# Kernel tuning notes

Measured on AMD Instinct MI355X. Metric: run time of the kernel, lower is better.

Reference implementation:

```python
import jax, jax.numpy as jnp
import numpy as np

B, S, H = 32, 1, 1024            # decode: one query token per sequence
NH, HD = 16, 64                  # num_heads, head_dim
BS = 16                          # cache block size
MAX_KV = 2048                    # max sequence length in cache
BLOCKS_PER_SEQ = MAX_KV // BS    # 128
NUM_BLOCKS = B * BLOCKS_PER_SEQ  # 4096 physical blocks
SCALE = HD ** -0.5


def setup_inputs() -> dict:
    key = jax.random.key(0)
    ks = jax.random.split(key, 8)
    hidden_states = jax.random.normal(ks[0], (B, S, H), jnp.float32) * 0.02
    # kv_cache[0] = key cache, kv_cache[1] = value cache; paged layout
    kv_cache = jax.random.normal(ks[1], (2, NUM_BLOCKS, BS, NH, HD), jnp.float32) * 0.02
    # each sequence owns a contiguous run of physical blocks (valid block table)
    block_tables = jnp.arange(NUM_BLOCKS, dtype=jnp.int32).reshape(B, BLOCKS_PER_SEQ)
    seq_lens = jax.random.randint(ks[2], (B,), 1, MAX_KV + 1, dtype=jnp.int32)
    w_attn = jax.random.normal(ks[3], (H, 3 * H), jnp.float32) * 0.02
    b_attn = jax.random.normal(ks[4], (3 * H,), jnp.float32) * 0.02
    w_proj = jax.random.normal(ks[5], (H, H), jnp.float32) * 0.02
    b_proj = jax.random.normal(ks[6], (H,), jnp.float32) * 0.02
    return {"hidden_states": hidden_states, "kv_cache": kv_cache,
            "block_tables": block_tables, "seq_lens": seq_lens,
            "w_attn": w_attn, "b_attn": b_attn,
            "w_proj": w_proj, "b_proj": b_proj}


def reference(hidden_states, kv_cache, block_tables, seq_lens,
              w_attn, b_attn, w_proj, b_proj):
    # qkv projection (c_attn); only q is consumed by the paged-attention decode
    qkv = hidden_states @ w_attn + b_attn                      # [B, S, 3H]
    q = qkv[..., :H].reshape(B, S, NH, HD)                     # [B, 1, NH, HD]

    # block-table gather of paged KV cache
    # kv_cache[0][block_tables]: [B, BLOCKS_PER_SEQ, BS, NH, HD]
    keys = kv_cache[0][block_tables].reshape(B, MAX_KV, NH, HD)
    vals = kv_cache[1][block_tables].reshape(B, MAX_KV, NH, HD)

    scores = jnp.einsum('bsnd,bknd->bnsk', q, keys) * SCALE    # [B, NH, S, MAX_KV]
    valid = jnp.arange(MAX_KV)[None, :] < seq_lens[:, None]    # [B, MAX_KV]
    scores = jnp.where(valid[:, None, None, :], scores, -jnp.inf)
    probs = jax.nn.softmax(scores, axis=-1)

    attn = jnp.einsum('bnsk,bknd->bsnd', probs, vals).reshape(B, S, H)
    return attn @ w_proj + b_proj                              # [B, S, H]
```

## Files before the change

kernel.cpp:

```cpp
#include <hip/hip_runtime.h>
#include <hip/hip_bf16.h>

#define BATCH 32
#define HID 1024
#define NH 16
#define HD 64
#define BS 16
#define MAX_KV 2048
#define BPS 128
#define NUM_BLOCKS 4096
#define SCALE 0.125f

#define SPLITS 16
#define CHUNK 128
#define KSPLIT 16
#define KCHUNK (HID / KSPLIT)

__global__ __launch_bounds__(256) void init_kernel(
    const float* __restrict__ b_attn, const float* __restrict__ b_proj,
    float* __restrict__ q, float* __restrict__ out)
{
    const int i = blockIdx.x * 256 + threadIdx.x;
    const int col = i & (HID - 1);
    q[i]   = b_attn[col];
    out[i] = b_proj[col];
}

__global__ __launch_bounds__(256) void gemv_kernel(
    const float* __restrict__ x,
    const float* __restrict__ w,
    float* __restrict__ y,
    int wstride)
{
    const int colg = blockIdx.x;
    const int kz = blockIdx.y;
    const int tid = threadIdx.x, wave = tid >> 6, lane = tid & 63;
    const int col = colg * 64 + lane;

    __shared__ __align__(16) float s_x[BATCH * KCHUNK];
    for (int i = tid; i < BATCH * KCHUNK; i += 256) {
        const int bb = i >> 6, kk = i & (KCHUNK - 1);
        s_x[i] = x[bb * HID + kz * KCHUNK + kk];
    }
    __syncthreads();

    const int b0 = wave * 8;
    float acc[8];
    #pragma unroll
    for (int b = 0; b < 8; ++b) acc[b] = 0.f;

    const float4* s_x4 = reinterpret_cast<const float4*>(s_x);
    const float* wp = w + (size_t)(kz * KCHUNK) * wstride + col;
    #pragma unroll
    for (int jb = 0; jb < KCHUNK / 4; ++jb) {
        const float wv0 = wp[(size_t)(jb * 4 + 0) * wstride];
        const float wv1 = wp[(size_t)(jb * 4 + 1) * wstride];
        const float wv2 = wp[(size_t)(jb * 4 + 2) * wstride];
        const float wv3 = wp[(size_t)(jb * 4 + 3) * wstride];
        #pragma unroll
        for (int b = 0; b < 8; ++b) {
            const float4 xv = s_x4[(b0 + b) * (KCHUNK / 4) + jb];
            acc[b] += xv.x * wv0 + xv.y * wv1 + xv.z * wv2 + xv.w * wv3;
        }
    }
    #pragma unroll
    for (int b = 0; b < 8; ++b)
        atomicAdd(&y[(size_t)(b0 + b) * HID + col], acc[b]);
}

__global__ __launch_bounds__(256) void attn_split_kernel(
    const float* __restrict__ q,
    const float* __restrict__ kv,
    const int* __restrict__ block_tables,
    const int* __restrict__ seq_lens,
    float* __restrict__ part)
{
    const int h = blockIdx.x, b = blockIdx.y, s = blockIdx.z;
    const int n = seq_lens[b];
    const int p0 = s * CHUNK;
    if (p0 >= n) return;
    const int cnt = min(n - p0, CHUNK);

    const int tid = threadIdx.x, wave = tid >> 6, lane = tid & 63;
    const int pos_sub = lane >> 4;
    const int d4 = lane & 15;

    float* my_part = part + ((size_t)(b * NH + h) * SPLITS + s) * (HD + 2);

    __shared__ float s_sc[CHUNK];
    __shared__ int   s_bt[CHUNK / BS];
    __shared__ float s_redm[4], s_redl[4];
    __shared__ float s_part[4 * HD];

    if (tid < CHUNK / BS) s_bt[tid] = block_tables[b * BPS + s * (CHUNK / BS) + tid];
    float4 qv = *reinterpret_cast<const float4*>(
        q + (size_t)(b * NH + h) * HD + d4 * 4);
    qv.x *= SCALE; qv.y *= SCALE; qv.z *= SCALE; qv.w *= SCALE;
    __syncthreads();

    const size_t v_off = (size_t)NUM_BLOCKS * BS * NH * HD;

    for (int base = wave * 16; base < cnt; base += 64) {
        float sc[4];
        #pragma unroll
        for (int u = 0; u < 4; ++u) {
            const int p = base + 4 * pos_sub + u;
            sc[u] = 0.f;
            if (p < cnt) {
                const float* kp = kv + (((size_t)s_bt[p >> 4] * BS + (p & 15)) * NH + h) * HD + d4 * 4;
                const float4 k4 = *reinterpret_cast<const float4*>(kp);
                sc[u] = qv.x * k4.x + qv.y * k4.y + qv.z * k4.z + qv.w * k4.w;
            }
        }
        #pragma unroll
        for (int u = 0; u < 4; ++u) {
            sc[u] += __shfl_xor(sc[u], 1);
            sc[u] += __shfl_xor(sc[u], 2);
            sc[u] += __shfl_xor(sc[u], 4);
            sc[u] += __shfl_xor(sc[u], 8);
            const int p = base + 4 * pos_sub + u;
            if (d4 == 0 && p < cnt) s_sc[p] = sc[u];
        }
    }
    __syncthreads();

    const float v = (tid < cnt) ? s_sc[tid] : -1e30f;
    float m = v;
    #pragma unroll
    for (int msk = 32; msk; msk >>= 1) m = fmaxf(m, __shfl_xor(m, msk));
    if (lane == 0) s_redm[wave] = m;
    __syncthreads();
    m = fmaxf(fmaxf(s_redm[0], s_redm[1]), fmaxf(s_redm[2], s_redm[3]));

    const float e = (tid < cnt) ? __expf(v - m) : 0.f;
    if (tid < cnt) s_sc[tid] = e;
    float l = e;
    #pragma unroll
    for (int msk = 32; msk; msk >>= 1) l += __shfl_xor(l, msk);
    if (lane == 0) s_redl[wave] = l;
    __syncthreads();
    const float l_tot = s_redl[0] + s_redl[1] + s_redl[2] + s_redl[3];

    float4 acc = {0.f, 0.f, 0.f, 0.f};
    for (int base = wave * 16; base < cnt; base += 64) {
        #pragma unroll
        for (int u = 0; u < 4; ++u) {
            const int p = base + 4 * pos_sub + u;
            if (p < cnt) {
                const float* vp = kv + v_off + (((size_t)s_bt[p >> 4] * BS + (p & 15)) * NH + h) * HD + d4 * 4;
                const float4 v4 = *reinterpret_cast<const float4*>(vp);
                const float w = s_sc[p];
                acc.x += w * v4.x; acc.y += w * v4.y;
                acc.z += w * v4.z; acc.w += w * v4.w;
            }
        }
    }
    acc.x += __shfl_xor(acc.x, 16); acc.y += __shfl_xor(acc.y, 16);
    acc.z += __shfl_xor(acc.z, 16); acc.w += __shfl_xor(acc.w, 16);
    acc.x += __shfl_xor(acc.x, 32); acc.y += __shfl_xor(acc.y, 32);
    acc.z += __shfl_xor(acc.z, 32); acc.w += __shfl_xor(acc.w, 32);
    if (pos_sub == 0) {
        s_part[wave * HD + d4 * 4 + 0] = acc.x;
        s_part[wave * HD + d4 * 4 + 1] = acc.y;
        s_part[wave * HD + d4 * 4 + 2] = acc.z;
        s_part[wave * HD + d4 * 4 + 3] = acc.w;
    }
    __syncthreads();
    if (tid < HD) {
        my_part[tid] = s_part[tid] + s_part[HD + tid] +
                       s_part[2 * HD + tid] + s_part[3 * HD + tid];
    }
    if (tid == 0) { my_part[HD] = m; my_part[HD + 1] = l_tot; }
}

__global__ __launch_bounds__(64) void attn_reduce_kernel(
    const float* __restrict__ part,
    const int* __restrict__ seq_lens,
    float* __restrict__ attn_out)
{
    const int h = blockIdx.x, b = blockIdx.y, d = threadIdx.x;
    const int n = seq_lens[b];
    const int ns = (n + CHUNK - 1) / CHUNK;
    const float* pp = part + (size_t)(b * NH + h) * SPLITS * (HD + 2);
    float m = -1e30f;
    for (int s = 0; s < ns; ++s) m = fmaxf(m, pp[s * (HD + 2) + HD]);
    float o = 0.f, l = 0.f;
    for (int s = 0; s < ns; ++s) {
        const float a = __expf(pp[s * (HD + 2) + HD] - m);
        o += a * pp[s * (HD + 2) + d];
        l += a * pp[s * (HD + 2) + HD + 1];
    }
    attn_out[(size_t)b * HID + h * HD + d] = o / l;
}

extern "C" void kernel_launch(void* const* d_in, const int* in_sizes, int n_in,
                              void* d_out, int out_size, void* d_ws, size_t ws_size,
                              hipStream_t stream) {
    const float* hs     = (const float*)d_in[0];
    const float* kv     = (const float*)d_in[1];
    const int*   bt     = (const int*)d_in[2];
    const int*   sl     = (const int*)d_in[3];
    const float* w_attn = (const float*)d_in[4];
    const float* b_attn = (const float*)d_in[5];
    const float* w_proj = (const float*)d_in[6];
    const float* b_proj = (const float*)d_in[7];
    float* out = (float*)d_out;

    float* q    = (float*)d_ws;
    float* attn = q + BATCH * HID;
    float* part = attn + BATCH * HID;

    init_kernel<<<BATCH * HID / 256, 256, 0, stream>>>(b_attn, b_proj, q, out);
    gemv_kernel<<<dim3(HID / 64, KSPLIT), 256, 0, stream>>>(hs, w_attn, q, 3 * HID);
    attn_split_kernel<<<dim3(NH, BATCH, SPLITS), 256, 0, stream>>>(q, kv, bt, sl, part);
    attn_reduce_kernel<<<dim3(NH, BATCH), 64, 0, stream>>>(part, sl, attn);
    gemv_kernel<<<dim3(HID / 64, KSPLIT), 256, 0, stream>>>(attn, w_proj, out, HID);
}
```

Measured before the change: 691.5 us.

## Fuse QK and PV passes in split attention with per-lane online softmax

```diff
diff --git a/kernel.cpp b/kernel.cpp
--- a/kernel.cpp
+++ b/kernel.cpp
@@ -87,10 +87,9 @@
 
     float* my_part = part + ((size_t)(b * NH + h) * SPLITS + s) * (HD + 2);
 
-    __shared__ float s_sc[CHUNK];
     __shared__ int   s_bt[CHUNK / BS];
-    __shared__ float s_redm[4], s_redl[4];
-    __shared__ float s_part[4 * HD];
+    __shared__ float s_m[4], s_l[4];
+    __shared__ float s_o[4 * HD];
 
     if (tid < CHUNK / BS) s_bt[tid] = block_tables[b * BPS + s * (CHUNK / BS) + tid];
     float4 qv = *reinterpret_cast<const float4*>(
@@ -100,15 +99,26 @@
 
     const size_t v_off = (size_t)NUM_BLOCKS * BS * NH * HD;
 
+    float m[4], l[4];
+    float4 acc[4];
+    #pragma unroll
+    for (int u = 0; u < 4; ++u) {
+        m[u] = -1e30f; l[u] = 0.f;
+        acc[u].x = acc[u].y = acc[u].z = acc[u].w = 0.f;
+    }
+
     for (int base = wave * 16; base < cnt; base += 64) {
         float sc[4];
+        float4 vv[4];
         #pragma unroll
         for (int u = 0; u < 4; ++u) {
-            const int p = base + 4 * pos_sub + u;
+            const int p = base + pos_sub * 4 + u;
             sc[u] = 0.f;
+            vv[u].x = vv[u].y = vv[u].z = vv[u].w = 0.f;
             if (p < cnt) {
-                const float* kp = kv + (((size_t)s_bt[p >> 4] * BS + (p & 15)) * NH + h) * HD + d4 * 4;
-                const float4 k4 = *reinterpret_cast<const float4*>(kp);
+                const size_t boff = (((size_t)s_bt[p >> 4] * BS + (p & 15)) * NH + h) * HD + d4 * 4;
+                const float4 k4 = *reinterpret_cast<const float4*>(kv + boff);
+                vv[u] = *reinterpret_cast<const float4*>(kv + v_off + boff);
                 sc[u] = qv.x * k4.x + qv.y * k4.y + qv.z * k4.z + qv.w * k4.w;
             }
         }
@@ -118,59 +128,68 @@
             sc[u] += __shfl_xor(sc[u], 2);
             sc[u] += __shfl_xor(sc[u], 4);
             sc[u] += __shfl_xor(sc[u], 8);
-            const int p = base + 4 * pos_sub + u;
-            if (d4 == 0 && p < cnt) s_sc[p] = sc[u];
-        }
-    }
-    __syncthreads();
-
-    const float v = (tid < cnt) ? s_sc[tid] : -1e30f;
-    float m = v;
-    #pragma unroll
-    for (int msk = 32; msk; msk >>= 1) m = fmaxf(m, __shfl_xor(m, msk));
-    if (lane == 0) s_redm[wave] = m;
-    __syncthreads();
-    m = fmaxf(fmaxf(s_redm[0], s_redm[1]), fmaxf(s_redm[2], s_redm[3]));
-
-    const float e = (tid < cnt) ? __expf(v - m) : 0.f;
-    if (tid < cnt) s_sc[tid] = e;
-    float l = e;
-    #pragma unroll
-    for (int msk = 32; msk; msk >>= 1) l += __shfl_xor(l, msk);
-    if (lane == 0) s_redl[wave] = l;
-    __syncthreads();
-    const float l_tot = s_redl[0] + s_redl[1] + s_redl[2] + s_redl[3];
-
-    float4 acc = {0.f, 0.f, 0.f, 0.f};
-    for (int base = wave * 16; base < cnt; base += 64) {
+        }
         #pragma unroll
         for (int u = 0; u < 4; ++u) {
-            const int p = base + 4 * pos_sub + u;
+            const int p = base + pos_sub * 4 + u;
             if (p < cnt) {
-                const float* vp = kv + v_off + (((size_t)s_bt[p >> 4] * BS + (p & 15)) * NH + h) * HD + d4 * 4;
-                const float4 v4 = *reinterpret_cast<const float4*>(vp);
-                const float w = s_sc[p];
-                acc.x += w * v4.x; acc.y += w * v4.y;
-                acc.z += w * v4.z; acc.w += w * v4.w;
+                const float mn = fmaxf(m[u], sc[u]);
+                const float sca = __expf(m[u] - mn);
+                const float f   = __expf(sc[u] - mn);
+                l[u] = l[u] * sca + f;
+                acc[u].x = acc[u].x * sca + f * vv[u].x;
+                acc[u].y = acc[u].y * sca + f * vv[u].y;
+                acc[u].z = acc[u].z * sca + f * vv[u].z;
+                acc[u].w = acc[u].w * sca + f * vv[u].w;
+                m[u] = mn;
             }
         }
     }
-    acc.x += __shfl_xor(acc.x, 16); acc.y += __shfl_xor(acc.y, 16);
-    acc.z += __shfl_xor(acc.z, 16); acc.w += __shfl_xor(acc.w, 16);
-    acc.x += __shfl_xor(acc.x, 32); acc.y += __shfl_xor(acc.y, 32);
-    acc.z += __shfl_xor(acc.z, 32); acc.w += __shfl_xor(acc.w, 32);
+
+    float mm = fmaxf(fmaxf(m[0], m[1]), fmaxf(m[2], m[3]));
+    const float a0 = __expf(m[0] - mm), a1 = __expf(m[1] - mm);
+    const float a2 = __expf(m[2] - mm), a3 = __expf(m[3] - mm);
+    float ll = l[0] * a0 + l[1] * a1 + l[2] * a2 + l[3] * a3;
+    float4 oo;
+    oo.x = acc[0].x * a0 + acc[1].x * a1 + acc[2].x * a2 + acc[3].x * a3;
+    oo.y = acc[0].y * a0 + acc[1].y * a1 + acc[2].y * a2 + acc[3].y * a3;
+    oo.z = acc[0].z * a0 + acc[1].z * a1 + acc[2].z * a2 + acc[3].z * a3;
+    oo.w = acc[0].w * a0 + acc[1].w * a1 + acc[2].w * a2 + acc[3].w * a3;
+
+    #pragma unroll
+    for (int msk = 16; msk <= 32; msk <<= 1) {
+        const float mo = __shfl_xor(mm, msk);
+        const float lo = __shfl_xor(ll, msk);
+        float4 ot;
+        ot.x = __shfl_xor(oo.x, msk); ot.y = __shfl_xor(oo.y, msk);
+        ot.z = __shfl_xor(oo.z, msk); ot.w = __shfl_xor(oo.w, msk);
+        const float mn = fmaxf(mm, mo);
+        const float sa = __expf(mm - mn), sb = __expf(mo - mn);
+        ll = ll * sa + lo * sb;
+        oo.x = oo.x * sa + ot.x * sb; oo.y = oo.y * sa + ot.y * sb;
+        oo.z = oo.z * sa + ot.z * sb; oo.w = oo.w * sa + ot.w * sb;
+        mm = mn;
+    }
+
     if (pos_sub == 0) {
-        s_part[wave * HD + d4 * 4 + 0] = acc.x;
-        s_part[wave * HD + d4 * 4 + 1] = acc.y;
-        s_part[wave * HD + d4 * 4 + 2] = acc.z;
-        s_part[wave * HD + d4 * 4 + 3] = acc.w;
+        s_o[wave * HD + d4 * 4 + 0] = oo.x;
+        s_o[wave * HD + d4 * 4 + 1] = oo.y;
+        s_o[wave * HD + d4 * 4 + 2] = oo.z;
+        s_o[wave * HD + d4 * 4 + 3] = oo.w;
+        if (d4 == 0) { s_m[wave] = mm; s_l[wave] = ll; }
     }
     __syncthreads();
     if (tid < HD) {
-        my_part[tid] = s_part[tid] + s_part[HD + tid] +
-                       s_part[2 * HD + tid] + s_part[3 * HD + tid];
-    }
-    if (tid == 0) { my_part[HD] = m; my_part[HD + 1] = l_tot; }
+        const float M = fmaxf(fmaxf(s_m[0], s_m[1]), fmaxf(s_m[2], s_m[3]));
+        const float w0 = __expf(s_m[0] - M), w1 = __expf(s_m[1] - M);
+        const float w2 = __expf(s_m[2] - M), w3 = __expf(s_m[3] - M);
+        my_part[tid] = s_o[tid] * w0 + s_o[HD + tid] * w1 +
+                       s_o[2 * HD + tid] * w2 + s_o[3 * HD + tid] * w3;
+        if (tid == 0) {
+            my_part[HD] = M;
+            my_part[HD + 1] = s_l[0] * w0 + s_l[1] * w1 + s_l[2] * w2 + s_l[3] * w3;
+        }
+    }
 }
 
 __global__ __launch_bounds__(64) void attn_reduce_kernel(
```

Measured after the change: 673.8 us. -2.6%, faster.
